# Kernel tuning notes

Measured on AMD Instinct MI355X. Metric: run time of the kernel, lower is better.

## Reference

```python
import jax, jax.numpy as jnp
import numpy as np

EMB_DIM = 512
N_HEADS = 8
HEAD_DIM = EMB_DIM // N_HEADS


def setup_inputs() -> dict:
    key = jax.random.key(0)
    k1, k2, k3, k4, k5 = jax.random.split(key, 5)
    B, S = 4, 2048
    x = jax.random.normal(k1, (B, S, EMB_DIM), dtype=jnp.float32)
    # nn.Linear params: weight [out, in], bias [out]
    W_qkv = jax.random.normal(k2, (3 * EMB_DIM, EMB_DIM), dtype=jnp.float32) * (EMB_DIM ** -0.5)
    b_qkv = jax.random.normal(k3, (3 * EMB_DIM,), dtype=jnp.float32) * 0.02
    W_out = jax.random.normal(k4, (EMB_DIM, EMB_DIM), dtype=jnp.float32) * (EMB_DIM ** -0.5)
    b_out = jax.random.normal(k5, (EMB_DIM,), dtype=jnp.float32) * 0.02
    return {"x": x, "W_qkv": W_qkv, "b_qkv": b_qkv, "W_out": W_out, "b_out": b_out}


def reference(x, W_qkv, b_qkv, W_out, b_out):
    B, S, E = x.shape
    scale = E ** (-0.5)  # note: scores are DIVIDED by this, i.e. multiplied by sqrt(E)
    qkv = x @ W_qkv.T + b_qkv                       # [B, S, 3E]
    qkv = qkv.reshape(B, S, N_HEADS, 3 * HEAD_DIM).transpose(0, 2, 1, 3)  # [B, H, S, 3d]
    q, k, v = jnp.split(qkv, 3, axis=-1)            # each [B, H, S, d]
    scores = jnp.einsum("bhqd,bhkd->bhqk", q, k) / scale
    attn = jax.nn.softmax(scores, axis=-1)
    attn = jax.nn.softmax(attn, axis=-1)            # double softmax, faithful to source
    o = jnp.einsum("bhqk,bhkd->bhqd", attn, v)      # [B, H, S, d]
    o = o.transpose(0, 2, 1, 3).reshape(B, S, E)
    return o @ W_out.T + b_out
```

## Files before the change

kernel.cpp:

```cpp
#include <hip/hip_runtime.h>

typedef __bf16 bf16;
typedef __attribute__((ext_vector_type(4))) __bf16 bf16x4;
typedef __attribute__((ext_vector_type(8))) __bf16 bf16x8;
typedef __attribute__((ext_vector_type(4))) float f32x4;

#define MFMA(A,B,C) __builtin_amdgcn_mfma_f32_16x16x32_bf16(A,B,C,0,0,0)

#define SEQ 2048
#define EMB 512
#define HD  64
#define SCALE 22.627416997969522f
#define NEG_SEED -3.0e4f
#define LCAP 24

__global__ __launch_bounds__(256)
void convert_kernel(const float* __restrict__ x, const float* __restrict__ Wqkv,
                    const float* __restrict__ Wout,
                    bf16* __restrict__ Xh, bf16* __restrict__ Xl,
                    bf16* __restrict__ Wqh, bf16* __restrict__ Wql,
                    bf16* __restrict__ Wo, float* __restrict__ Vs) {
  if (blockIdx.x < 8) Vs[blockIdx.x * 256 + threadIdx.x] = 0.f;
  const int NX = 8192 * 512 / 4;
  const int NW = 1536 * 512 / 4;
  const int NO = 512 * 512 / 4;
  const int stride = gridDim.x * 256;
  for (int i = blockIdx.x * 256 + threadIdx.x; i < NX + NW + NO; i += stride) {
    const float* src; bf16 *dh, *dl; int j; bool haslo;
    if (i < NX)           { src = x;    dh = Xh;  dl = Xl;  j = i;           haslo = true; }
    else if (i < NX + NW) { src = Wqkv; dh = Wqh; dl = Wql; j = i - NX;      haslo = true; }
    else                  { src = Wout; dh = Wo;  dl = Wo;  j = i - NX - NW; haslo = false; }
    f32x4 v = *(const f32x4*)&src[(size_t)j * 4];
    bf16x4 h4, l4;
#pragma unroll
    for (int r = 0; r < 4; ++r) {
      bf16 h = (bf16)v[r]; h4[r] = h; l4[r] = (bf16)(v[r] - (float)h);
    }
    *(bf16x4*)&dh[(size_t)j * 4] = h4;
    if (haslo) *(bf16x4*)&dl[(size_t)j * 4] = l4;
  }
}

__global__ __launch_bounds__(256)
void gemm_qkv(const bf16* __restrict__ Xh, const bf16* __restrict__ Xl,
              const bf16* __restrict__ Wh, const bf16* __restrict__ Wl,
              const float* __restrict__ bias,
              bf16* __restrict__ Qh, bf16* __restrict__ Ql,
              bf16* __restrict__ Kh, bf16* __restrict__ Kl,
              bf16* __restrict__ Vrm, float* __restrict__ Vs) {
  __shared__ __align__(16) bf16 Ah[64][64], Al[64][64];
  __shared__ __align__(16) bf16 Bh[64][64], Bl[64][64];
  const int tid  = threadIdx.x;
  const int lane = tid & 63, wave = tid >> 6;
  const int lin = blockIdx.x + gridDim.x * blockIdx.y;
  const int xcd = lin & 7;
  const int w_  = lin >> 3;
  const int m0 = ((w_ & 15) + xcd * 16) * 64;
  const int n0 = (w_ >> 4) * 64;
  const bool isV = ((n0 % 192) == 128);
  const int wm = (wave >> 1) * 32, wn = (wave & 1) * 32;
  const int c = lane & 15, quad = lane >> 4;
  const int sr   = tid >> 3;
  const int scol = (tid & 7) * 8;
  const int sphy = ((tid & 7) ^ (sr & 7)) * 8;

  const f32x4 zero = {0.f, 0.f, 0.f, 0.f};
  f32x4 acc[2][2];
  acc[0][0] = zero; acc[0][1] = zero; acc[1][0] = zero; acc[1][1] = zero;

  for (int k0 = 0; k0 < 512; k0 += 64) {
    *(bf16x8*)&Ah[sr][sphy]      = *(const bf16x8*)&Xh[(size_t)(m0 + sr     ) * 512 + k0 + scol];
    *(bf16x8*)&Ah[sr + 32][sphy] = *(const bf16x8*)&Xh[(size_t)(m0 + sr + 32) * 512 + k0 + scol];
    *(bf16x8*)&Bh[sr][sphy]      = *(const bf16x8*)&Wh[(size_t)(n0 + sr     ) * 512 + k0 + scol];
    *(bf16x8*)&Bh[sr + 32][sphy] = *(const bf16x8*)&Wh[(size_t)(n0 + sr + 32) * 512 + k0 + scol];
    if (!isV) {
      *(bf16x8*)&Al[sr][sphy]      = *(const bf16x8*)&Xl[(size_t)(m0 + sr     ) * 512 + k0 + scol];
      *(bf16x8*)&Al[sr + 32][sphy] = *(const bf16x8*)&Xl[(size_t)(m0 + sr + 32) * 512 + k0 + scol];
      *(bf16x8*)&Bl[sr][sphy]      = *(const bf16x8*)&Wl[(size_t)(n0 + sr     ) * 512 + k0 + scol];
      *(bf16x8*)&Bl[sr + 32][sphy] = *(const bf16x8*)&Wl[(size_t)(n0 + sr + 32) * 512 + k0 + scol];
    }
    __syncthreads();
#pragma unroll
    for (int ks = 0; ks < 64; ks += 32) {
      const int px = (((ks >> 3) + quad) ^ (c & 7)) * 8;
      bf16x8 ah0 = *(bf16x8*)&Ah[wm + c     ][px];
      bf16x8 ah1 = *(bf16x8*)&Ah[wm + 16 + c][px];
      bf16x8 bh0 = *(bf16x8*)&Bh[wn + c     ][px];
      bf16x8 bh1 = *(bf16x8*)&Bh[wn + 16 + c][px];
      if (isV) {
        acc[0][0] = MFMA(ah0, bh0, acc[0][0]);
        acc[0][1] = MFMA(ah0, bh1, acc[0][1]);
        acc[1][0] = MFMA(ah1, bh0, acc[1][0]);
        acc[1][1] = MFMA(ah1, bh1, acc[1][1]);
      } else {
        bf16x8 al0 = *(bf16x8*)&Al[wm + c     ][px];
        bf16x8 al1 = *(bf16x8*)&Al[wm + 16 + c][px];
        bf16x8 bl0 = *(bf16x8*)&Bl[wn + c     ][px];
        bf16x8 bl1 = *(bf16x8*)&Bl[wn + 16 + c][px];
        acc[0][0] = MFMA(ah0, bh0, acc[0][0]);
        acc[0][0] = MFMA(al0, bh0, acc[0][0]);
        acc[0][0] = MFMA(ah0, bl0, acc[0][0]);
        acc[0][1] = MFMA(ah0, bh1, acc[0][1]);
        acc[0][1] = MFMA(al0, bh1, acc[0][1]);
        acc[0][1] = MFMA(ah0, bl1, acc[0][1]);
        acc[1][0] = MFMA(ah1, bh0, acc[1][0]);
        acc[1][0] = MFMA(al1, bh0, acc[1][0]);
        acc[1][0] = MFMA(ah1, bl0, acc[1][0]);
        acc[1][1] = MFMA(ah1, bh1, acc[1][1]);
        acc[1][1] = MFMA(al1, bh1, acc[1][1]);
        acc[1][1] = MFMA(ah1, bl1, acc[1][1]);
      }
    }
    __syncthreads();
  }

  if (isV) {
#pragma unroll
    for (int nt = 0; nt < 2; ++nt) {
      const int n = n0 + wn + nt * 16 + c;
      const float bv = bias[n];
      const int h = n / 192, d = n % 192 - 128;
      const size_t bh = (size_t)((m0 >> 11) * 8 + h);
      float csum = 0.f;
#pragma unroll
      for (int mt = 0; mt < 2; ++mt)
#pragma unroll
        for (int r = 0; r < 4; ++r) {
          const int m = m0 + wm + mt * 16 + quad * 4 + r;
          const int s = m & 2047;
          float v = acc[mt][nt][r] + bv;
          Vrm[(bh * SEQ + s) * HD + d] = (bf16)v;
          csum += v;
        }
      csum += __shfl_xor(csum, 16, 64);
      csum += __shfl_xor(csum, 32, 64);
      if (quad == 0) atomicAdd(&Vs[bh * HD + d], csum);
    }
  } else {
#pragma unroll
    for (int mt = 0; mt < 2; ++mt) {
#pragma unroll
      for (int nt = 0; nt < 2; ++nt) {
        const int n = n0 + wn + nt * 16 + c;
        const float bv = bias[n];
#pragma unroll
        for (int r = 0; r < 4; ++r) {
          const int m = m0 + wm + mt * 16 + quad * 4 + r;
          float v = acc[mt][nt][r] + bv;
          const int h = n / 192, t = n % 192;
          const size_t bh = (size_t)((m >> 11) * 8 + h);
          const int s = m & 2047;
          if (t < 64) {
            float q = v * SCALE;
            bf16 hi = (bf16)q;
            float lo = q - (float)hi;
            size_t idx = (bh * SEQ + s) * HD + t;
            Qh[idx] = hi; Ql[idx] = (bf16)lo;
          } else {
            bf16 hi = (bf16)v;
            float lo = v - (float)hi;
            size_t idx = (bh * SEQ + s) * HD + (t - 64);
            Kh[idx] = hi; Kl[idx] = (bf16)lo;
          }
        }
      }
    }
  }
}

__global__ __launch_bounds__(256)
void gemm_out(const bf16* __restrict__ A, const bf16* __restrict__ Wo,
              const float* __restrict__ bias, float* __restrict__ C) {
  __shared__ __align__(16) bf16 As[64][64];
  __shared__ __align__(16) bf16 Bs[64][64];
  const int tid  = threadIdx.x;
  const int lane = tid & 63, wave = tid >> 6;
  const int lin = blockIdx.x + gridDim.x * blockIdx.y;
  const int xcd = lin & 7;
  const int w_  = lin >> 3;
  const int m0 = ((w_ & 15) + xcd * 16) * 64;
  const int n0 = (w_ >> 4) * 64;
  const int wm = (wave >> 1) * 32, wn = (wave & 1) * 32;
  const int c = lane & 15, quad = lane >> 4;
  const int sr   = tid >> 3;
  const int scol = (tid & 7) * 8;
  const int sphy = ((tid & 7) ^ (sr & 7)) * 8;

  const f32x4 zero = {0.f, 0.f, 0.f, 0.f};
  f32x4 acc[2][2];
  acc[0][0] = zero; acc[0][1] = zero; acc[1][0] = zero; acc[1][1] = zero;

  for (int k0 = 0; k0 < 512; k0 += 64) {
    *(bf16x8*)&As[sr][sphy]      = *(const bf16x8*)&A [(size_t)(m0 + sr     ) * 512 + k0 + scol];
    *(bf16x8*)&As[sr + 32][sphy] = *(const bf16x8*)&A [(size_t)(m0 + sr + 32) * 512 + k0 + scol];
    *(bf16x8*)&Bs[sr][sphy]      = *(const bf16x8*)&Wo[(size_t)(n0 + sr     ) * 512 + k0 + scol];
    *(bf16x8*)&Bs[sr + 32][sphy] = *(const bf16x8*)&Wo[(size_t)(n0 + sr + 32) * 512 + k0 + scol];
    __syncthreads();
#pragma unroll
    for (int ks = 0; ks < 64; ks += 32) {
      const int px = (((ks >> 3) + quad) ^ (c & 7)) * 8;
      bf16x8 a0 = *(bf16x8*)&As[wm + c     ][px];
      bf16x8 a1 = *(bf16x8*)&As[wm + 16 + c][px];
      bf16x8 b0 = *(bf16x8*)&Bs[wn + c     ][px];
      bf16x8 b1 = *(bf16x8*)&Bs[wn + 16 + c][px];
      acc[0][0] = MFMA(a0, b0, acc[0][0]);
      acc[0][1] = MFMA(a0, b1, acc[0][1]);
      acc[1][0] = MFMA(a1, b0, acc[1][0]);
      acc[1][1] = MFMA(a1, b1, acc[1][1]);
    }
    __syncthreads();
  }

#pragma unroll
  for (int mt = 0; mt < 2; ++mt) {
#pragma unroll
    for (int nt = 0; nt < 2; ++nt) {
      const int n = n0 + wn + nt * 16 + c;
      const float bv = bias[n];
#pragma unroll
      for (int r = 0; r < 4; ++r) {
        const int m = m0 + wm + mt * 16 + quad * 4 + r;
        C[(size_t)m * 512 + n] = acc[mt][nt][r] + bv;
      }
    }
  }
}

__global__ __launch_bounds__(256, 4)
void attn_kernel(const bf16* __restrict__ Qh, const bf16* __restrict__ Ql,
                 const bf16* __restrict__ Kh, const bf16* __restrict__ Kl,
                 const bf16* __restrict__ Vrm, const float* __restrict__ Vs,
                 bf16* __restrict__ O) {
  __shared__ __align__(16) bf16 SK[2][64][64];
  __shared__ float sS[4][16][LCAP];
  __shared__ unsigned short sI[4][16][LCAP];
  __shared__ int pcnt[4][16];

  const int tid  = threadIdx.x;
  const int lane = tid & 63, wave = tid >> 6;
  const int c = lane & 15, quad = lane >> 4;
  const int bh = blockIdx.x;
  const int q0 = blockIdx.y * 64 + wave * 16;
  const size_t hoff = (size_t)bh * SEQ * HD;
  const bf16* qh_p = Qh + hoff;
  const bf16* ql_p = Ql + hoff;
  const bf16* kh_p = Kh + hoff;
  const bf16* kl_p = Kl + hoff;
  const bf16* v_p  = Vrm + hoff;
  const f32x4 zero = {0.f, 0.f, 0.f, 0.f};

  const int sr   = tid >> 3;
  const int scol = (tid & 7) * 8;
  const int sphy = ((tid & 7) ^ (sr & 7)) * 8;
  const int pc0  = ((0 + quad) ^ (c & 7)) * 8;
  const int pc1  = ((4 + quad) ^ (c & 7)) * 8;

  bf16x8 qf[2], qlf[2];
#pragma unroll
  for (int t = 0; t < 2; ++t) {
    size_t off = (size_t)(q0 + c) * HD + t * 32 + quad * 8;
    qf[t]  = *(const bf16x8*)&qh_p[off];
    qlf[t] = *(const bf16x8*)&ql_p[off];
  }
  if (lane < 16) pcnt[wave][lane] = 0;

  bf16x8 pA = *(const bf16x8*)&kh_p[(size_t)(sr     ) * HD + scol];
  bf16x8 pB = *(const bf16x8*)&kh_p[(size_t)(sr + 32) * HD + scol];
  *(bf16x8*)&SK[0][sr     ][sphy] = pA;
  *(bf16x8*)&SK[0][sr + 32][sphy] = pB;
  __syncthreads();

  float mr = NEG_SEED;
  int buf = 0;
  for (int cs = 0; cs < 32; ++cs) {
    if (cs < 31) {
      const size_t k0 = (size_t)(cs + 1) * 64;
      pA = *(const bf16x8*)&kh_p[(k0 + sr     ) * HD + scol];
      pB = *(const bf16x8*)&kh_p[(k0 + sr + 32) * HD + scol];
    }
#pragma unroll
    for (int t = 0; t < 4; ++t) {
      const int g = cs * 4 + t;
      bf16x8 kh0 = *(bf16x8*)&SK[buf][t * 16 + c][pc0];
      bf16x8 kh1 = *(bf16x8*)&SK[buf][t * 16 + c][pc1];
      f32x4 sc = MFMA(kh0, qf[0], zero);
      sc = MFMA(kh1, qf[1], sc);
      const float tm = fmaxf(fmaxf(sc[0], sc[1]), fmaxf(sc[2], sc[3]));
      mr = fmaxf(mr, tm);
      if (t & 1) {
        mr = fmaxf(mr, __shfl_xor(mr, 16, 64));
        mr = fmaxf(mr, __shfl_xor(mr, 32, 64));
      }
      if (tm > mr - 12.f) {
#pragma unroll
        for (int r = 0; r < 4; ++r) {
          if (sc[r] > mr - 12.f) {
            const int slot = atomicAdd(&pcnt[wave][c], 1) % LCAP;
            sI[wave][c][slot] = (unsigned short)(g * 16 + quad * 4 + r);
          }
        }
      }
    }
    if (cs < 31) {
      const int nb = buf ^ 1;
      *(bf16x8*)&SK[nb][sr     ][sphy] = pA;
      *(bf16x8*)&SK[nb][sr + 32][sphy] = pB;
      __syncthreads();
      buf = nb;
    }
  }

  float qv[16];
#pragma unroll
  for (int j = 0; j < 8; ++j) {
    qv[j]     = (float)qf[0][j] + (float)qlf[0][j];
    qv[8 + j] = (float)qf[1][j] + (float)qlf[1][j];
  }
  const int n = min(pcnt[wave][c], LCAP);
  float mqC = NEG_SEED;
  for (int j = 0; j < n; ++j) {
    const int idx = sI[wave][c][j];
    const size_t kr = (size_t)idx * HD + quad * 8;
    bf16x8 kh0 = *(const bf16x8*)&kh_p[kr];
    bf16x8 kh1 = *(const bf16x8*)&kh_p[kr + 32];
    bf16x8 kl0 = *(const bf16x8*)&kl_p[kr];
    bf16x8 kl1 = *(const bf16x8*)&kl_p[kr + 32];
    float s = 0.f;
#pragma unroll
    for (int jj = 0; jj < 8; ++jj) {
      s = fmaf(qv[jj],     (float)kh0[jj] + (float)kl0[jj], s);
      s = fmaf(qv[8 + jj], (float)kh1[jj] + (float)kl1[jj], s);
    }
    s += __shfl_xor(s, 16, 64);
    s += __shfl_xor(s, 32, 64);
    if (quad == 0) sS[wave][c][j] = s;
    mqC = fmaxf(mqC, s);
  }
  float l1 = 0.f;
  for (int j = 0; j < n; ++j) l1 += __expf(sS[wave][c][j] - mqC);
  const float inv1 = 1.f / l1;

  float oc[16];
#pragma unroll
  for (int i = 0; i < 16; ++i) oc[i] = 0.f;
  float l2 = 0.f;
  for (int j = 0; j < n; ++j) {
    const float a1 = __expf(sS[wave][c][j] - mqC) * inv1;
    const float t1 = __expf(a1) - 1.0f;
    l2 += t1;
    const int idx = sI[wave][c][j];
    bf16x8 v0 = *(const bf16x8*)&v_p[(size_t)idx * HD + quad * 8];
    bf16x8 v1 = *(const bf16x8*)&v_p[(size_t)idx * HD + 32 + quad * 8];
#pragma unroll
    for (int jj = 0; jj < 8; ++jj) {
      oc[jj]     += t1 * (float)v0[jj];
      oc[8 + jj] += t1 * (float)v1[jj];
    }
  }

  const int b = bh >> 3, h = bh & 7;
  const float rcp = 1.f / (2048.f + l2);
  const float* vsp = Vs + bh * HD;
  bf16* orow = &O[((size_t)b * SEQ + q0 + c) * EMB + h * HD];
  bf16x8 o0, o1;
#pragma unroll
  for (int jj = 0; jj < 8; ++jj) {
    o0[jj] = (bf16)((oc[jj]     + vsp[quad * 8 + jj])      * rcp);
    o1[jj] = (bf16)((oc[8 + jj] + vsp[32 + quad * 8 + jj]) * rcp);
  }
  *(bf16x8*)&orow[quad * 8]      = o0;
  *(bf16x8*)&orow[32 + quad * 8] = o1;
}

extern "C" void kernel_launch(void* const* d_in, const int* in_sizes, int n_in,
                              void* d_out, int out_size, void* d_ws, size_t ws_size,
                              hipStream_t stream) {
  const float* x    = (const float*)d_in[0];
  const float* Wqkv = (const float*)d_in[1];
  const float* bqkv = (const float*)d_in[2];
  const float* Wout = (const float*)d_in[3];
  const float* bout = (const float*)d_in[4];
  float* out = (float*)d_out;

  char* ws = (char*)d_ws;
  const size_t SZ = (size_t)32 * SEQ * HD * 2;
  bf16* Qh  = (bf16*)(ws + 0 * SZ);
  bf16* Ql  = (bf16*)(ws + 1 * SZ);
  bf16* Kh  = (bf16*)(ws + 2 * SZ);
  bf16* Kl  = (bf16*)(ws + 3 * SZ);
  bf16* Vrm = (bf16*)(ws + 4 * SZ);
  bf16* XhO = (bf16*)(ws + 5 * SZ);
  bf16* Xl  = (bf16*)(ws + 6 * SZ);
  bf16* Wqh = (bf16*)(ws + 7 * SZ);
  bf16* Wql = (bf16*)(ws + 7 * SZ + 0x180000);
  bf16* Wo  = (bf16*)(ws + 7 * SZ + 0x300000);
  float* Vs = (float*)(ws + 7 * SZ + 0x380000);

  convert_kernel<<<dim3(2048), 256, 0, stream>>>(x, Wqkv, Wout, XhO, Xl, Wqh, Wql, Wo, Vs);
  gemm_qkv<<<dim3(128, 24), 256, 0, stream>>>(XhO, Xl, Wqh, Wql, bqkv, Qh, Ql, Kh, Kl, Vrm, Vs);
  attn_kernel<<<dim3(32, 32), 256, 0, stream>>>(Qh, Ql, Kh, Kl, Vrm, Vs, XhO);
  gemm_out<<<dim3(128, 8), 256, 0, stream>>>(XhO, Wo, bout, out);
}
```

Before: 194.7 us.

## Enlarge QKV GEMM tile and process two query tiles per attention wave

The QKV GEMM now uses 128x64 block tiles with each wave covering 32 rows by the full 64 columns, which halves the grid and increases reuse of the B tile. The attention kernel processes 32 query rows per wave (two 16-row sets), so every K tile staged in shared memory feeds twice as many MFMAs. It also moves the running-max cross-lane reduction to once per chunk and shrinks the candidate cap from 24 to 16. These changes aim to cut redundant K loading and launch overhead, at the cost of more registers and lower occupancy. The smaller candidate cap, together with the less frequent max refresh, raises the risk of dropping or overwriting candidate keys.

```diff
diff --git a/kernel.cpp b/kernel.cpp
--- a/kernel.cpp
+++ b/kernel.cpp
@@ -12,7 +12,7 @@
 #define HD  64
 #define SCALE 22.627416997969522f
 #define NEG_SEED -3.0e4f
-#define LCAP 24
+#define LCAP 16
 
 __global__ __launch_bounds__(256)
 void convert_kernel(const float* __restrict__ x, const float* __restrict__ Wqkv,
@@ -41,43 +41,50 @@
   }
 }
 
-__global__ __launch_bounds__(256)
+__global__ __launch_bounds__(256, 3)
 void gemm_qkv(const bf16* __restrict__ Xh, const bf16* __restrict__ Xl,
               const bf16* __restrict__ Wh, const bf16* __restrict__ Wl,
               const float* __restrict__ bias,
               bf16* __restrict__ Qh, bf16* __restrict__ Ql,
               bf16* __restrict__ Kh, bf16* __restrict__ Kl,
               bf16* __restrict__ Vrm, float* __restrict__ Vs) {
-  __shared__ __align__(16) bf16 Ah[64][64], Al[64][64];
-  __shared__ __align__(16) bf16 Bh[64][64], Bl[64][64];
+  __shared__ __align__(16) bf16 Ah[128][64], Al[128][64];
+  __shared__ __align__(16) bf16 Bh[64][64],  Bl[64][64];
   const int tid  = threadIdx.x;
   const int lane = tid & 63, wave = tid >> 6;
-  const int lin = blockIdx.x + gridDim.x * blockIdx.y;
+  const int lin = blockIdx.x;
   const int xcd = lin & 7;
   const int w_  = lin >> 3;
-  const int m0 = ((w_ & 15) + xcd * 16) * 64;
-  const int n0 = (w_ >> 4) * 64;
+  const int m0 = ((w_ & 7) + xcd * 8) * 128;
+  const int n0 = (w_ >> 3) * 64;
   const bool isV = ((n0 % 192) == 128);
-  const int wm = (wave >> 1) * 32, wn = (wave & 1) * 32;
+  const int wm = wave * 32;
   const int c = lane & 15, quad = lane >> 4;
   const int sr   = tid >> 3;
   const int scol = (tid & 7) * 8;
   const int sphy = ((tid & 7) ^ (sr & 7)) * 8;
 
   const f32x4 zero = {0.f, 0.f, 0.f, 0.f};
-  f32x4 acc[2][2];
-  acc[0][0] = zero; acc[0][1] = zero; acc[1][0] = zero; acc[1][1] = zero;
+  f32x4 acc[2][4];
+#pragma unroll
+  for (int mt = 0; mt < 2; ++mt)
+#pragma unroll
+    for (int nt = 0; nt < 4; ++nt) acc[mt][nt] = zero;
 
   for (int k0 = 0; k0 < 512; k0 += 64) {
-    *(bf16x8*)&Ah[sr][sphy]      = *(const bf16x8*)&Xh[(size_t)(m0 + sr     ) * 512 + k0 + scol];
-    *(bf16x8*)&Ah[sr + 32][sphy] = *(const bf16x8*)&Xh[(size_t)(m0 + sr + 32) * 512 + k0 + scol];
-    *(bf16x8*)&Bh[sr][sphy]      = *(const bf16x8*)&Wh[(size_t)(n0 + sr     ) * 512 + k0 + scol];
-    *(bf16x8*)&Bh[sr + 32][sphy] = *(const bf16x8*)&Wh[(size_t)(n0 + sr + 32) * 512 + k0 + scol];
+    *(bf16x8*)&Ah[sr      ][sphy] = *(const bf16x8*)&Xh[(size_t)(m0 + sr      ) * 512 + k0 + scol];
+    *(bf16x8*)&Ah[sr + 32 ][sphy] = *(const bf16x8*)&Xh[(size_t)(m0 + sr + 32 ) * 512 + k0 + scol];
+    *(bf16x8*)&Ah[sr + 64 ][sphy] = *(const bf16x8*)&Xh[(size_t)(m0 + sr + 64 ) * 512 + k0 + scol];
+    *(bf16x8*)&Ah[sr + 96 ][sphy] = *(const bf16x8*)&Xh[(size_t)(m0 + sr + 96 ) * 512 + k0 + scol];
+    *(bf16x8*)&Bh[sr      ][sphy] = *(const bf16x8*)&Wh[(size_t)(n0 + sr      ) * 512 + k0 + scol];
+    *(bf16x8*)&Bh[sr + 32 ][sphy] = *(const bf16x8*)&Wh[(size_t)(n0 + sr + 32 ) * 512 + k0 + scol];
     if (!isV) {
-      *(bf16x8*)&Al[sr][sphy]      = *(const bf16x8*)&Xl[(size_t)(m0 + sr     ) * 512 + k0 + scol];
-      *(bf16x8*)&Al[sr + 32][sphy] = *(const bf16x8*)&Xl[(size_t)(m0 + sr + 32) * 512 + k0 + scol];
-      *(bf16x8*)&Bl[sr][sphy]      = *(const bf16x8*)&Wl[(size_t)(n0 + sr     ) * 512 + k0 + scol];
-      *(bf16x8*)&Bl[sr + 32][sphy] = *(const bf16x8*)&Wl[(size_t)(n0 + sr + 32) * 512 + k0 + scol];
+      *(bf16x8*)&Al[sr      ][sphy] = *(const bf16x8*)&Xl[(size_t)(m0 + sr      ) * 512 + k0 + scol];
+      *(bf16x8*)&Al[sr + 32 ][sphy] = *(const bf16x8*)&Xl[(size_t)(m0 + sr + 32 ) * 512 + k0 + scol];
+      *(bf16x8*)&Al[sr + 64 ][sphy] = *(const bf16x8*)&Xl[(size_t)(m0 + sr + 64 ) * 512 + k0 + scol];
+      *(bf16x8*)&Al[sr + 96 ][sphy] = *(const bf16x8*)&Xl[(size_t)(m0 + sr + 96 ) * 512 + k0 + scol];
+      *(bf16x8*)&Bl[sr      ][sphy] = *(const bf16x8*)&Wl[(size_t)(n0 + sr      ) * 512 + k0 + scol];
+      *(bf16x8*)&Bl[sr + 32 ][sphy] = *(const bf16x8*)&Wl[(size_t)(n0 + sr + 32 ) * 512 + k0 + scol];
     }
     __syncthreads();
 #pragma unroll
@@ -85,30 +92,30 @@
       const int px = (((ks >> 3) + quad) ^ (c & 7)) * 8;
       bf16x8 ah0 = *(bf16x8*)&Ah[wm + c     ][px];
       bf16x8 ah1 = *(bf16x8*)&Ah[wm + 16 + c][px];
-      bf16x8 bh0 = *(bf16x8*)&Bh[wn + c     ][px];
-      bf16x8 bh1 = *(bf16x8*)&Bh[wn + 16 + c][px];
+      bf16x8 bh[4];
+#pragma unroll
+      for (int nt = 0; nt < 4; ++nt) bh[nt] = *(bf16x8*)&Bh[nt * 16 + c][px];
       if (isV) {
-        acc[0][0] = MFMA(ah0, bh0, acc[0][0]);
-        acc[0][1] = MFMA(ah0, bh1, acc[0][1]);
-        acc[1][0] = MFMA(ah1, bh0, acc[1][0]);
-        acc[1][1] = MFMA(ah1, bh1, acc[1][1]);
+#pragma unroll
+        for (int nt = 0; nt < 4; ++nt) {
+          acc[0][nt] = MFMA(ah0, bh[nt], acc[0][nt]);
+          acc[1][nt] = MFMA(ah1, bh[nt], acc[1][nt]);
+        }
       } else {
         bf16x8 al0 = *(bf16x8*)&Al[wm + c     ][px];
         bf16x8 al1 = *(bf16x8*)&Al[wm + 16 + c][px];
-        bf16x8 bl0 = *(bf16x8*)&Bl[wn + c     ][px];
-        bf16x8 bl1 = *(bf16x8*)&Bl[wn + 16 + c][px];
-        acc[0][0] = MFMA(ah0, bh0, acc[0][0]);
-        acc[0][0] = MFMA(al0, bh0, acc[0][0]);
-        acc[0][0] = MFMA(ah0, bl0, acc[0][0]);
-        acc[0][1] = MFMA(ah0, bh1, acc[0][1]);
-        acc[0][1] = MFMA(al0, bh1, acc[0][1]);
-        acc[0][1] = MFMA(ah0, bl1, acc[0][1]);
-        acc[1][0] = MFMA(ah1, bh0, acc[1][0]);
-        acc[1][0] = MFMA(al1, bh0, acc[1][0]);
-        acc[1][0] = MFMA(ah1, bl0, acc[1][0]);
-        acc[1][1] = MFMA(ah1, bh1, acc[1][1]);
-        acc[1][1] = MFMA(al1, bh1, acc[1][1]);
-        acc[1][1] = MFMA(ah1, bl1, acc[1][1]);
+        bf16x8 bl[4];
+#pragma unroll
+        for (int nt = 0; nt < 4; ++nt) bl[nt] = *(bf16x8*)&Bl[nt * 16 + c][px];
+#pragma unroll
+        for (int nt = 0; nt < 4; ++nt) {
+          acc[0][nt] = MFMA(ah0, bh[nt], acc[0][nt]);
+          acc[0][nt] = MFMA(al0, bh[nt], acc[0][nt]);
+          acc[0][nt] = MFMA(ah0, bl[nt], acc[0][nt]);
+          acc[1][nt] = MFMA(ah1, bh[nt], acc[1][nt]);
+          acc[1][nt] = MFMA(al1, bh[nt], acc[1][nt]);
+          acc[1][nt] = MFMA(ah1, bl[nt], acc[1][nt]);
+        }
       }
     }
     __syncthreads();
@@ -116,11 +123,11 @@
 
   if (isV) {
 #pragma unroll
-    for (int nt = 0; nt < 2; ++nt) {
-      const int n = n0 + wn + nt * 16 + c;
+    for (int nt = 0; nt < 4; ++nt) {
+      const int n = n0 + nt * 16 + c;
       const float bv = bias[n];
       const int h = n / 192, d = n % 192 - 128;
-      const size_t bh = (size_t)((m0 >> 11) * 8 + h);
+      const size_t bh_ = (size_t)((m0 >> 11) * 8 + h);
       float csum = 0.f;
 #pragma unroll
       for (int mt = 0; mt < 2; ++mt)
@@ -129,37 +136,37 @@
           const int m = m0 + wm + mt * 16 + quad * 4 + r;
           const int s = m & 2047;
           float v = acc[mt][nt][r] + bv;
-          Vrm[(bh * SEQ + s) * HD + d] = (bf16)v;
+          Vrm[(bh_ * SEQ + s) * HD + d] = (bf16)v;
           csum += v;
         }
       csum += __shfl_xor(csum, 16, 64);
       csum += __shfl_xor(csum, 32, 64);
-      if (quad == 0) atomicAdd(&Vs[bh * HD + d], csum);
+      if (quad == 0) atomicAdd(&Vs[bh_ * HD + d], csum);
     }
   } else {
 #pragma unroll
     for (int mt = 0; mt < 2; ++mt) {
 #pragma unroll
-      for (int nt = 0; nt < 2; ++nt) {
-        const int n = n0 + wn + nt * 16 + c;
+      for (int nt = 0; nt < 4; ++nt) {
+        const int n = n0 + nt * 16 + c;
         const float bv = bias[n];
 #pragma unroll
         for (int r = 0; r < 4; ++r) {
           const int m = m0 + wm + mt * 16 + quad * 4 + r;
           float v = acc[mt][nt][r] + bv;
           const int h = n / 192, t = n % 192;
-          const size_t bh = (size_t)((m >> 11) * 8 + h);
+          const size_t bh_ = (size_t)((m >> 11) * 8 + h);
           const int s = m & 2047;
           if (t < 64) {
             float q = v * SCALE;
             bf16 hi = (bf16)q;
             float lo = q - (float)hi;
-            size_t idx = (bh * SEQ + s) * HD + t;
+            size_t idx = (bh_ * SEQ + s) * HD + t;
             Qh[idx] = hi; Ql[idx] = (bf16)lo;
           } else {
             bf16 hi = (bf16)v;
             float lo = v - (float)hi;
-            size_t idx = (bh * SEQ + s) * HD + (t - 64);
+            size_t idx = (bh_ * SEQ + s) * HD + (t - 64);
             Kh[idx] = hi; Kl[idx] = (bf16)lo;
           }
         }
@@ -226,21 +233,21 @@
   }
 }
 
-__global__ __launch_bounds__(256, 4)
+__global__ __launch_bounds__(256, 2)
 void attn_kernel(const bf16* __restrict__ Qh, const bf16* __restrict__ Ql,
                  const bf16* __restrict__ Kh, const bf16* __restrict__ Kl,
                  const bf16* __restrict__ Vrm, const float* __restrict__ Vs,
                  bf16* __restrict__ O) {
   __shared__ __align__(16) bf16 SK[2][64][64];
-  __shared__ float sS[4][16][LCAP];
-  __shared__ unsigned short sI[4][16][LCAP];
-  __shared__ int pcnt[4][16];
+  __shared__ float sS[4][32][LCAP];
+  __shared__ unsigned short sI[4][32][LCAP];
+  __shared__ int pcnt[4][32];
 
   const int tid  = threadIdx.x;
   const int lane = tid & 63, wave = tid >> 6;
   const int c = lane & 15, quad = lane >> 4;
   const int bh = blockIdx.x;
-  const int q0 = blockIdx.y * 64 + wave * 16;
+  const int q0 = blockIdx.y * 128 + wave * 32;
   const size_t hoff = (size_t)bh * SEQ * HD;
   const bf16* qh_p = Qh + hoff;
   const bf16* ql_p = Ql + hoff;
@@ -255,14 +262,17 @@
   const int pc0  = ((0 + quad) ^ (c & 7)) * 8;
   const int pc1  = ((4 + quad) ^ (c & 7)) * 8;
 
-  bf16x8 qf[2], qlf[2];
+  bf16x8 qfA[2], qlfA[2], qfB[2], qlfB[2];
 #pragma unroll
   for (int t = 0; t < 2; ++t) {
-    size_t off = (size_t)(q0 + c) * HD + t * 32 + quad * 8;
-    qf[t]  = *(const bf16x8*)&qh_p[off];
-    qlf[t] = *(const bf16x8*)&ql_p[off];
-  }
-  if (lane < 16) pcnt[wave][lane] = 0;
+    size_t offA = (size_t)(q0 + c) * HD + t * 32 + quad * 8;
+    size_t offB = (size_t)(q0 + 16 + c) * HD + t * 32 + quad * 8;
+    qfA[t]  = *(const bf16x8*)&qh_p[offA];
+    qlfA[t] = *(const bf16x8*)&ql_p[offA];
+    qfB[t]  = *(const bf16x8*)&qh_p[offB];
+    qlfB[t] = *(const bf16x8*)&ql_p[offB];
+  }
+  if (lane < 32) pcnt[wave][lane] = 0;
 
   bf16x8 pA = *(const bf16x8*)&kh_p[(size_t)(sr     ) * HD + scol];
   bf16x8 pB = *(const bf16x8*)&kh_p[(size_t)(sr + 32) * HD + scol];
@@ -270,7 +280,7 @@
   *(bf16x8*)&SK[0][sr + 32][sphy] = pB;
   __syncthreads();
 
-  float mr = NEG_SEED;
+  float mrA = NEG_SEED, mrB = NEG_SEED;
   int buf = 0;
   for (int cs = 0; cs < 32; ++cs) {
     if (cs < 31) {
@@ -283,24 +293,35 @@
       const int g = cs * 4 + t;
       bf16x8 kh0 = *(bf16x8*)&SK[buf][t * 16 + c][pc0];
       bf16x8 kh1 = *(bf16x8*)&SK[buf][t * 16 + c][pc1];
-      f32x4 sc = MFMA(kh0, qf[0], zero);
-      sc = MFMA(kh1, qf[1], sc);
-      const float tm = fmaxf(fmaxf(sc[0], sc[1]), fmaxf(sc[2], sc[3]));
-      mr = fmaxf(mr, tm);
-      if (t & 1) {
-        mr = fmaxf(mr, __shfl_xor(mr, 16, 64));
-        mr = fmaxf(mr, __shfl_xor(mr, 32, 64));
-      }
-      if (tm > mr - 12.f) {
-#pragma unroll
-        for (int r = 0; r < 4; ++r) {
-          if (sc[r] > mr - 12.f) {
-            const int slot = atomicAdd(&pcnt[wave][c], 1) % LCAP;
+      f32x4 sA = MFMA(kh0, qfA[0], zero);
+      sA = MFMA(kh1, qfA[1], sA);
+      f32x4 sB = MFMA(kh0, qfB[0], zero);
+      sB = MFMA(kh1, qfB[1], sB);
+      const float tmA = fmaxf(fmaxf(sA[0], sA[1]), fmaxf(sA[2], sA[3]));
+      const float tmB = fmaxf(fmaxf(sB[0], sB[1]), fmaxf(sB[2], sB[3]));
+      mrA = fmaxf(mrA, tmA);
+      mrB = fmaxf(mrB, tmB);
+      if (tmA > mrA - 12.f) {
+#pragma unroll
+        for (int r = 0; r < 4; ++r)
+          if (sA[r] > mrA - 12.f) {
+            const int slot = atomicAdd(&pcnt[wave][c], 1) & (LCAP - 1);
             sI[wave][c][slot] = (unsigned short)(g * 16 + quad * 4 + r);
           }
-        }
       }
-    }
+      if (tmB > mrB - 12.f) {
+#pragma unroll
+        for (int r = 0; r < 4; ++r)
+          if (sB[r] > mrB - 12.f) {
+            const int slot = atomicAdd(&pcnt[wave][16 + c], 1) & (LCAP - 1);
+            sI[wave][16 + c][slot] = (unsigned short)(g * 16 + quad * 4 + r);
+          }
+      }
+    }
+    mrA = fmaxf(mrA, __shfl_xor(mrA, 16, 64));
+    mrA = fmaxf(mrA, __shfl_xor(mrA, 32, 64));
+    mrB = fmaxf(mrB, __shfl_xor(mrB, 16, 64));
+    mrB = fmaxf(mrB, __shfl_xor(mrB, 32, 64));
     if (cs < 31) {
       const int nb = buf ^ 1;
       *(bf16x8*)&SK[nb][sr     ][sphy] = pA;
@@ -310,66 +331,71 @@
     }
   }
 
-  float qv[16];
-#pragma unroll
-  for (int j = 0; j < 8; ++j) {
-    qv[j]     = (float)qf[0][j] + (float)qlf[0][j];
-    qv[8 + j] = (float)qf[1][j] + (float)qlf[1][j];
-  }
-  const int n = min(pcnt[wave][c], LCAP);
-  float mqC = NEG_SEED;
-  for (int j = 0; j < n; ++j) {
-    const int idx = sI[wave][c][j];
-    const size_t kr = (size_t)idx * HD + quad * 8;
-    bf16x8 kh0 = *(const bf16x8*)&kh_p[kr];
-    bf16x8 kh1 = *(const bf16x8*)&kh_p[kr + 32];
-    bf16x8 kl0 = *(const bf16x8*)&kl_p[kr];
-    bf16x8 kl1 = *(const bf16x8*)&kl_p[kr + 32];
-    float s = 0.f;
-#pragma unroll
-    for (int jj = 0; jj < 8; ++jj) {
-      s = fmaf(qv[jj],     (float)kh0[jj] + (float)kl0[jj], s);
-      s = fmaf(qv[8 + jj], (float)kh1[jj] + (float)kl1[jj], s);
-    }
-    s += __shfl_xor(s, 16, 64);
-    s += __shfl_xor(s, 32, 64);
-    if (quad == 0) sS[wave][c][j] = s;
-    mqC = fmaxf(mqC, s);
-  }
-  float l1 = 0.f;
-  for (int j = 0; j < n; ++j) l1 += __expf(sS[wave][c][j] - mqC);
-  const float inv1 = 1.f / l1;
-
-  float oc[16];
-#pragma unroll
-  for (int i = 0; i < 16; ++i) oc[i] = 0.f;
-  float l2 = 0.f;
-  for (int j = 0; j < n; ++j) {
-    const float a1 = __expf(sS[wave][c][j] - mqC) * inv1;
-    const float t1 = __expf(a1) - 1.0f;
-    l2 += t1;
-    const int idx = sI[wave][c][j];
-    bf16x8 v0 = *(const bf16x8*)&v_p[(size_t)idx * HD + quad * 8];
-    bf16x8 v1 = *(const bf16x8*)&v_p[(size_t)idx * HD + 32 + quad * 8];
-#pragma unroll
-    for (int jj = 0; jj < 8; ++jj) {
-      oc[jj]     += t1 * (float)v0[jj];
-      oc[8 + jj] += t1 * (float)v1[jj];
-    }
-  }
-
   const int b = bh >> 3, h = bh & 7;
-  const float rcp = 1.f / (2048.f + l2);
   const float* vsp = Vs + bh * HD;
-  bf16* orow = &O[((size_t)b * SEQ + q0 + c) * EMB + h * HD];
-  bf16x8 o0, o1;
-#pragma unroll
-  for (int jj = 0; jj < 8; ++jj) {
-    o0[jj] = (bf16)((oc[jj]     + vsp[quad * 8 + jj])      * rcp);
-    o1[jj] = (bf16)((oc[8 + jj] + vsp[32 + quad * 8 + jj]) * rcp);
-  }
-  *(bf16x8*)&orow[quad * 8]      = o0;
-  *(bf16x8*)&orow[32 + quad * 8] = o1;
+
+#define FINISH_Q(LQ, QF, QLF, QROW) do {                                      \
+    float qv[16];                                                             \
+    _Pragma("unroll")                                                         \
+    for (int j = 0; j < 8; ++j) {                                             \
+      qv[j]     = (float)QF[0][j] + (float)QLF[0][j];                         \
+      qv[8 + j] = (float)QF[1][j] + (float)QLF[1][j];                         \
+    }                                                                         \
+    const int n = min(pcnt[wave][LQ], LCAP);                                  \
+    float mqC = NEG_SEED;                                                     \
+    for (int j = 0; j < n; ++j) {                                             \
+      const int idx = sI[wave][LQ][j];                                        \
+      const size_t kr = (size_t)idx * HD + quad * 8;                          \
+      bf16x8 kh0 = *(const bf16x8*)&kh_p[kr];                                 \
+      bf16x8 kh1 = *(const bf16x8*)&kh_p[kr + 32];                            \
+      bf16x8 kl0 = *(const bf16x8*)&kl_p[kr];                                 \
+      bf16x8 kl1 = *(const bf16x8*)&kl_p[kr + 32];                            \
+      float s = 0.f;                                                          \
+      _Pragma("unroll")                                                       \
+      for (int jj = 0; jj < 8; ++jj) {                                        \
+        s = fmaf(qv[jj],     (float)kh0[jj] + (float)kl0[jj], s);             \
+        s = fmaf(qv[8 + jj], (float)kh1[jj] + (float)kl1[jj], s);             \
+      }                                                                       \
+      s += __shfl_xor(s, 16, 64);                                             \
+      s += __shfl_xor(s, 32, 64);                                             \
+      if (quad == 0) sS[wave][LQ][j] = s;                                     \
+      mqC = fmaxf(mqC, s);                                                    \
+    }                                                                         \
+    float l1 = 0.f;                                                           \
+    for (int j = 0; j < n; ++j) l1 += __expf(sS[wave][LQ][j] - mqC);          \
+    const float inv1 = 1.f / l1;                                              \
+    float oc[16];                                                             \
+    _Pragma("unroll")                                                         \
+    for (int i = 0; i < 16; ++i) oc[i] = 0.f;                                 \
+    float l2 = 0.f;                                                           \
+    for (int j = 0; j < n; ++j) {                                             \
+      const float a1 = __expf(sS[wave][LQ][j] - mqC) * inv1;                  \
+      const float t1 = __expf(a1) - 1.0f;                                     \
+      l2 += t1;                                                               \
+      const int idx = sI[wave][LQ][j];                                        \
+      bf16x8 v0 = *(const bf16x8*)&v_p[(size_t)idx * HD + quad * 8];          \
+      bf16x8 v1 = *(const bf16x8*)&v_p[(size_t)idx * HD + 32 + quad * 8];     \
+      _Pragma("unroll")                                                       \
+      for (int jj = 0; jj < 8; ++jj) {                                        \
+        oc[jj]     += t1 * (float)v0[jj];                                     \
+        oc[8 + jj] += t1 * (float)v1[jj];                                     \
+      }                                                                       \
+    }                                                                         \
+    const float rcp = 1.f / (2048.f + l2);                                    \
+    bf16* orow = &O[((size_t)b * SEQ + (QROW)) * EMB + h * HD];               \
+    bf16x8 o0, o1;                                                            \
+    _Pragma("unroll")                                                         \
+    for (int jj = 0; jj < 8; ++jj) {                                          \
+      o0[jj] = (bf16)((oc[jj]     + vsp[quad * 8 + jj])      * rcp);          \
+      o1[jj] = (bf16)((oc[8 + jj] + vsp[32 + quad * 8 + jj]) * rcp);          \
+    }                                                                         \
+    *(bf16x8*)&orow[quad * 8]      = o0;                                      \
+    *(bf16x8*)&orow[32 + quad * 8] = o1;                                      \
+  } while (0)
+
+  FINISH_Q(c,      qfA, qlfA, q0 + c);
+  FINISH_Q(16 + c, qfB, qlfB, q0 + 16 + c);
+#undef FINISH_Q
 }
 
 extern "C" void kernel_launch(void* const* d_in, const int* in_sizes, int n_in,
@@ -397,7 +423,7 @@
   float* Vs = (float*)(ws + 7 * SZ + 0x380000);
 
   convert_kernel<<<dim3(2048), 256, 0, stream>>>(x, Wqkv, Wout, XhO, Xl, Wqh, Wql, Wo, Vs);
-  gemm_qkv<<<dim3(128, 24), 256, 0, stream>>>(XhO, Xl, Wqh, Wql, bqkv, Qh, Ql, Kh, Kl, Vrm, Vs);
-  attn_kernel<<<dim3(32, 32), 256, 0, stream>>>(Qh, Ql, Kh, Kl, Vrm, Vs, XhO);
+  gemm_qkv<<<dim3(1536), 256, 0, stream>>>(XhO, Xl, Wqh, Wql, bqkv, Qh, Ql, Kh, Kl, Vrm, Vs);
+  attn_kernel<<<dim3(32, 16), 256, 0, stream>>>(Qh, Ql, Kh, Kl, Vrm, Vs, XhO);
   gemm_out<<<dim3(128, 8), 256, 0, stream>>>(XhO, Wo, bout, out);
 }
```

Measured after the change: 209.1 us. 1.07x slower.
